# Performance work log

Measured on AMD Instinct MI355X. Metric: run time of the kernel, lower is better.

## Reference

```python
import jax, jax.numpy as jnp
import numpy as np

EMBED = 1024
B, S = 8, 2048

def setup_inputs() -> dict:
    key = jax.random.key(0)
    k1, k2 = jax.random.split(key)
    x = jax.random.normal(k1, (B, S, EMBED), dtype=jnp.float32)
    # torch Linear(embed, 3*embed): store weight already transposed as [E, 3E]
    W_qkv = jax.random.normal(k2, (EMBED, 3 * EMBED), dtype=jnp.float32) * (1.0 / np.sqrt(EMBED))
    b_qkv = jnp.zeros((3 * EMBED,), dtype=jnp.float32)
    return {"x": x, "W_qkv": W_qkv, "b_qkv": b_qkv}

def reference(x, W_qkv, b_qkv):
    E = x.shape[-1]
    qkv = x @ W_qkv + b_qkv                      # [B,S,3E]
    Q, K, V = jnp.split(qkv, 3, axis=-1)         # each [B,S,E]
    scale = 1.0 / jnp.sqrt(jnp.asarray(E, x.dtype))
    scores = jnp.einsum('bqe,bke->bqk', Q, K) * scale  # [B,S,S]
    attn = jax.nn.softmax(scores, axis=-1)
    return jnp.einsum('bqk,bke->bqe', attn, V)   # [B,S,E]
```

## Files before the change

### kernel.cpp

```cpp
#include <hip/hip_runtime.h>

typedef unsigned short u16;
typedef unsigned int u32;
typedef __attribute__((ext_vector_type(8))) short short8;
typedef __attribute__((ext_vector_type(4))) short short4v;
typedef __attribute__((ext_vector_type(4))) float f32x4;

__device__ __forceinline__ u16 f2bf(float f) {
    u32 u = __float_as_uint(f);
    u32 r = (u + 0x7fffu + ((u >> 16) & 1u)) >> 16;
    return (u16)r;
}
__device__ __forceinline__ float bf2f(u16 h) {
    return __uint_as_float(((u32)h) << 16);
}

__device__ __forceinline__ void gload_lds16(const void* g, void* l) {
    __builtin_amdgcn_global_load_lds((const __attribute__((address_space(1))) void*)g,
                                     (__attribute__((address_space(3))) void*)l, 16, 0, 0);
}

#define BARRIER() do { __builtin_amdgcn_sched_barrier(0); __builtin_amdgcn_s_barrier(); __builtin_amdgcn_sched_barrier(0); } while (0)
#define VMCNT(N)  asm volatile("s_waitcnt vmcnt(" #N ")" ::: "memory")


__device__ __forceinline__ void stage_half(const u16* __restrict__ gtile, int ldg, int kcol0,
                                           char* lds, int regionOff, int r0,
                                           int wid, int lane)
{
    const int cc = kcol0 + (((lane & 7) ^ (lane >> 3)) << 3);
    #pragma unroll
    for (int j = 0; j < 2; ++j) {
        const int rbase = r0 + j * 64 + (wid << 3);
        gload_lds16(gtile + (size_t)(rbase + (lane >> 3)) * ldg + cc,
                    lds + regionOff + (size_t)rbase * 128);
    }
}

template<int ROFF, int QH>
__device__ __forceinline__ void ld_a(short8 (&a)[4][2], const char* lds, int arow, const int colk[2]) {
    #pragma unroll
    for (int mf = 0; mf < 4; ++mf)
        #pragma unroll
        for (int kh = 0; kh < 2; ++kh)
            a[mf][kh] = *(const short8*)(lds + ROFF + QH * 16384 + mf * 2048 + arow + colk[kh]);
}
template<int ROFF, int QH>
__device__ __forceinline__ void ld_b(short8 (&b)[2][2], const char* lds, int brow, const int colk[2]) {
    #pragma unroll
    for (int nf = 0; nf < 2; ++nf)
        #pragma unroll
        for (int kh = 0; kh < 2; ++kh)
            b[nf][kh] = *(const short8*)(lds + ROFF + QH * 16384 + nf * 2048 + brow + colk[kh]);
}

template<int QM, int QN>
__device__ __forceinline__ void mfq(f32x4 (&acc)[2][4][2][2], short8 (&a)[4][2], short8 (&b)[2][2]) {
    __builtin_amdgcn_s_setprio(1);
    #pragma unroll
    for (int mf = 0; mf < 4; ++mf)
        #pragma unroll
        for (int nf = 0; nf < 2; ++nf) {
            acc[QM][mf][QN][nf] = __builtin_amdgcn_mfma_f32_16x16x32_bf16(a[mf][0], b[nf][0], acc[QM][mf][QN][nf], 0, 0, 0);
            acc[QM][mf][QN][nf] = __builtin_amdgcn_mfma_f32_16x16x32_bf16(a[mf][1], b[nf][1], acc[QM][mf][QN][nf], 0, 0, 0);
        }
    __builtin_amdgcn_s_setprio(0);
}

template<int EPI>
__global__ __launch_bounds__(512, 2)
void gemm8p(const u16* __restrict__ A, int lda, long long sA,
            const u16* __restrict__ B, int ldb, long long sB,
            void* __restrict__ Cv, int ldc, long long sC,
            const float* __restrict__ bias, float scale, int K)
{
    extern __shared__ char lds[];
    const int tid  = threadIdx.x;
    const int wid  = tid >> 6;
    const int lane = tid & 63;
    const long long z = blockIdx.z;

    const int bm = blockIdx.y * 256;
    const int bn = blockIdx.x * 256;
    const u16* Atile = A + z * sA + (size_t)bm * lda;
    const u16* Btile = B + z * sB + (size_t)bn * ldb;

    const int wm = wid >> 2;
    const int wn = wid & 3;

    const int l15  = lane & 15;
    const int lxor = (lane & 7) << 4;
    const int khi  = (lane >> 4) << 4;
    const int colk[2] = { khi ^ lxor, (64 + khi) ^ lxor };
    const int arow = (wm * 64 + l15) * 128;
    const int brow = (wn * 32 + l15) * 128;

    f32x4 acc[2][4][2][2];
    #pragma unroll
    for (int i = 0; i < 2; ++i)
        #pragma unroll
        for (int m = 0; m < 4; ++m)
            #pragma unroll
            for (int j = 0; j < 2; ++j)
                #pragma unroll
                for (int n = 0; n < 2; ++n)
                    acc[i][m][j][n] = (f32x4){0.f, 0.f, 0.f, 0.f};

    const int NT = K >> 6;
    const int NI = NT >> 1;

    stage_half(Atile, lda, 0,  lds, 0,     0,   wid, lane);
    stage_half(Btile, ldb, 0,  lds, 32768, 0,   wid, lane);
    stage_half(Atile, lda, 0,  lds, 0,     128, wid, lane);
    stage_half(Btile, ldb, 0,  lds, 32768, 128, wid, lane);
    stage_half(Atile, lda, 64, lds, 65536, 0,   wid, lane);
    stage_half(Btile, ldb, 64, lds, 98304, 0,   wid, lane);
    VMCNT(4);
    BARRIER();

    short8 a[4][2], b[2][2];

    for (int it = 0; it < NI; ++it) {
        const int k1 = (2 * it + 1) << 6;
        const int k2 = (2 * it + 2) << 6;
        const int k3 = (2 * it + 3) << 6;
        const bool lastit = (it == NI - 1);

        ld_a<0, 0>(a, lds, arow, colk);
        ld_b<32768, 0>(b, lds, brow, colk);
        stage_half(Atile, lda, k1, lds, 65536, 128, wid, lane);
        BARRIER(); mfq<0, 0>(acc, a, b); BARRIER();
        ld_b<32768, 1>(b, lds, brow, colk);
        stage_half(Btile, ldb, k1, lds, 98304, 128, wid, lane);
        BARRIER(); mfq<0, 1>(acc, a, b); BARRIER();
        ld_a<0, 1>(a, lds, arow, colk);
        ld_b<32768, 0>(b, lds, brow, colk);
        if (!lastit) stage_half(Atile, lda, k2, lds, 0, 0, wid, lane);
        BARRIER(); mfq<1, 0>(acc, a, b); BARRIER();
        ld_b<32768, 1>(b, lds, brow, colk);
        if (!lastit) { stage_half(Btile, ldb, k2, lds, 32768, 0, wid, lane); VMCNT(4); }
        else         { VMCNT(0); }
        BARRIER(); mfq<1, 1>(acc, a, b); BARRIER();
        ld_a<65536, 0>(a, lds, arow, colk);
        ld_b<98304, 0>(b, lds, brow, colk);
        if (!lastit) stage_half(Atile, lda, k2, lds, 0, 128, wid, lane);
        BARRIER(); mfq<0, 0>(acc, a, b); BARRIER();
        ld_b<98304, 1>(b, lds, brow, colk);
        if (!lastit) stage_half(Btile, ldb, k2, lds, 32768, 128, wid, lane);
        BARRIER(); mfq<0, 1>(acc, a, b); BARRIER();
        ld_a<65536, 1>(a, lds, arow, colk);
        ld_b<98304, 0>(b, lds, brow, colk);
        if (!lastit) stage_half(Atile, lda, k3, lds, 65536, 0, wid, lane);
        BARRIER(); mfq<1, 0>(acc, a, b); BARRIER();
        ld_b<98304, 1>(b, lds, brow, colk);
        if (!lastit) { stage_half(Btile, ldb, k3, lds, 98304, 0, wid, lane); VMCNT(4); }
        BARRIER(); mfq<1, 1>(acc, a, b); BARRIER();
    }

    const int r0 = (lane >> 4) * 4;
    const int cc = lane & 15;
    #pragma unroll
    for (int qn = 0; qn < 2; ++qn)
        #pragma unroll
        for (int nf = 0; nf < 2; ++nf) {
            const int col = bn + qn * 128 + wn * 32 + nf * 16 + cc;
            const float badd = (EPI == 0) ? bias[col] : 0.f;
            #pragma unroll
            for (int qm = 0; qm < 2; ++qm)
                #pragma unroll
                for (int mf = 0; mf < 4; ++mf) {
                    const int row = bm + qm * 128 + wm * 64 + mf * 16 + r0;
                    #pragma unroll
                    for (int r = 0; r < 4; ++r) {
                        const float v = acc[qm][mf][qn][nf][r] * scale + badd;
                        if (EPI == 2) ((float*)Cv + z * sC)[(size_t)(row + r) * ldc + col] = v;
                        else          ((u16*)Cv + z * sC)[(size_t)(row + r) * ldc + col] = f2bf(v);
                    }
                }
        }
}

__global__ __launch_bounds__(256)
void cvt_f32_bf16(const float* __restrict__ in, u16* __restrict__ out, int n8)
{
    const int i = blockIdx.x * 256 + threadIdx.x;
    if (i >= n8) return;
    const float4* p = (const float4*)in;
    const float4 a = p[2 * i], b = p[2 * i + 1];
    short8 o;
    o[0] = (short)f2bf(a.x); o[1] = (short)f2bf(a.y);
    o[2] = (short)f2bf(a.z); o[3] = (short)f2bf(a.w);
    o[4] = (short)f2bf(b.x); o[5] = (short)f2bf(b.y);
    o[6] = (short)f2bf(b.z); o[7] = (short)f2bf(b.w);
    ((short8*)out)[i] = o;
}

__global__ __launch_bounds__(256)
void cvt_w_t(const float* __restrict__ W, u16* __restrict__ Wt)
{
    __shared__ u16 T[32][33];
    const int tid = threadIdx.x;
    const int tr = tid >> 3;
    const int tc = (tid & 7) * 4;
    const int c0 = blockIdx.x * 32;
    const int r0 = blockIdx.y * 32;
    const float4 v = *(const float4*)&W[(size_t)(r0 + tr) * 3072 + c0 + tc];
    T[tr][tc + 0] = f2bf(v.x); T[tr][tc + 1] = f2bf(v.y);
    T[tr][tc + 2] = f2bf(v.z); T[tr][tc + 3] = f2bf(v.w);
    __syncthreads();
    short4v o;
    o[0] = (short)T[tc + 0][tr]; o[1] = (short)T[tc + 1][tr];
    o[2] = (short)T[tc + 2][tr]; o[3] = (short)T[tc + 3][tr];
    *(short4v*)&Wt[(size_t)(c0 + tr) * 1024 + r0 + tc] = o;
}

__global__ __launch_bounds__(256)
void trans_v(const u16* __restrict__ qkv, u16* __restrict__ Vt)
{
    __shared__ u16 T[32][33];
    const int tid = threadIdx.x;
    const int tr = tid >> 3;
    const int tc = (tid & 7) * 4;
    const int e0 = blockIdx.x * 32;
    const int s0 = blockIdx.y * 32;
    const int b  = blockIdx.z;
    const short4v v = *(const short4v*)&qkv[(size_t)(b * 2048 + s0 + tr) * 3072 + 2048 + e0 + tc];
    T[tr][tc + 0] = (u16)v[0]; T[tr][tc + 1] = (u16)v[1];
    T[tr][tc + 2] = (u16)v[2]; T[tr][tc + 3] = (u16)v[3];
    __syncthreads();
    short4v o;
    o[0] = (short)T[tc + 0][tr]; o[1] = (short)T[tc + 1][tr];
    o[2] = (short)T[tc + 2][tr]; o[3] = (short)T[tc + 3][tr];
    *(short4v*)&Vt[(size_t)b * 1024 * 2048 + (size_t)(e0 + tr) * 2048 + s0 + tc] = o;
}

__global__ __launch_bounds__(256)
void softmax_bf16(u16* __restrict__ S)
{
    u16* row = S + (size_t)blockIdx.x * 2048;
    const int tid  = threadIdx.x;
    const int wid  = tid >> 6;
    const int lane = tid & 63;
    __shared__ float red[4];

    const short8 v8 = *(const short8*)&row[tid * 8];
    float v[8];
    float m = -3.4e38f;
    #pragma unroll
    for (int j = 0; j < 8; ++j) { v[j] = bf2f((u16)v8[j]); m = fmaxf(m, v[j]); }
    #pragma unroll
    for (int off = 32; off; off >>= 1) m = fmaxf(m, __shfl_xor(m, off));
    if (lane == 0) red[wid] = m;
    __syncthreads();
    m = fmaxf(fmaxf(red[0], red[1]), fmaxf(red[2], red[3]));
    float s = 0.f;
    #pragma unroll
    for (int j = 0; j < 8; ++j) { v[j] = __expf(v[j] - m); s += v[j]; }
    #pragma unroll
    for (int off = 32; off; off >>= 1) s += __shfl_xor(s, off);
    __syncthreads();
    if (lane == 0) red[wid] = s;
    __syncthreads();
    s = red[0] + red[1] + red[2] + red[3];
    const float inv = 1.f / s;
    short8 o;
    #pragma unroll
    for (int j = 0; j < 8; ++j) o[j] = (short)f2bf(v[j] * inv);
    *(short8*)&row[tid * 8] = o;
}

extern "C" void kernel_launch(void* const* d_in, const int* in_sizes, int n_in,
                              void* d_out, int out_size, void* d_ws, size_t ws_size,
                              hipStream_t stream) {
    const float* x    = (const float*)d_in[0];
    const float* W    = (const float*)d_in[1];
    const float* bias = (const float*)d_in[2];
    float* out = (float*)d_out;

    const int B = 8, S = 2048, E = 1024, N3 = 3072;
    const int M = B * S;

    char* ws = (char*)d_ws;
    u16* xb   = (u16*)ws;
    u16* Wtb  = (u16*)(ws + 33554432);
    u16* qkvb = (u16*)(ws + 39845888);
    u16* Vtb  = (u16*)(ws + 140509184);
    u16* Sb   = (u16*)(ws + 174063616);

    const size_t need_full = 174063616ull + (size_t)B * S * S * 2;
    const bool full = ws_size >= need_full;
    const float sc = 1.0f / 32.0f;
    const int LDSB = 131072;

    (void)hipFuncSetAttribute(reinterpret_cast<const void*>(&gemm8p<0>),
                              hipFuncAttributeMaxDynamicSharedMemorySize, LDSB);
    (void)hipFuncSetAttribute(reinterpret_cast<const void*>(&gemm8p<1>),
                              hipFuncAttributeMaxDynamicSharedMemorySize, LDSB);
    (void)hipFuncSetAttribute(reinterpret_cast<const void*>(&gemm8p<2>),
                              hipFuncAttributeMaxDynamicSharedMemorySize, LDSB);

    cvt_f32_bf16<<<dim3((M * E) / 8 / 256), 256, 0, stream>>>(x, xb, (M * E) / 8);
    cvt_w_t<<<dim3(96, 32), 256, 0, stream>>>(W, Wtb);

    gemm8p<0><<<dim3(N3 / 256, M / 256, 1), 512, LDSB, stream>>>(
        xb, E, 0, Wtb, E, 0, qkvb, N3, 0, bias, 1.0f, E);

    trans_v<<<dim3(32, 64, 8), 256, 0, stream>>>(qkvb, Vtb);

    if (full) {
        gemm8p<1><<<dim3(S / 256, S / 256, 8), 512, LDSB, stream>>>(
            qkvb, N3, (long long)S * N3, qkvb + E, N3, (long long)S * N3,
            Sb, S, (long long)S * S, nullptr, sc, E);
        softmax_bf16<<<dim3(B * S), 256, 0, stream>>>(Sb);
        gemm8p<2><<<dim3(E / 256, S / 256, 8), 512, LDSB, stream>>>(
            Sb, S, (long long)S * S, Vtb, S, (long long)E * S,
            out, E, (long long)S * E, nullptr, 1.0f, S);
    } else {
        for (int b = 0; b < B; ++b) {
            const u16* Qb = qkvb + (size_t)b * S * N3;
            gemm8p<1><<<dim3(S / 256, S / 256, 1), 512, LDSB, stream>>>(
                Qb, N3, 0, Qb + E, N3, 0, Sb, S, 0, nullptr, sc, E);
            softmax_bf16<<<dim3(S), 256, 0, stream>>>(Sb);
            gemm8p<2><<<dim3(E / 256, S / 256, 1), 512, LDSB, stream>>>(
                Sb, S, 0, Vtb + (size_t)b * E * S, S, 0,
                out + (size_t)b * S * E, E, 0, nullptr, 1.0f, S);
        }
    }
}
```

Before: 314.0 us.

## Rework GEMM prefetch schedule, template strides, and remap blocks across XCDs

The GEMM kernel's K-loop is restructured so each iteration covers 128 K and prefetches a whole 64-K stage at once (deeper vmcnt(8)). It keeps two B fragment registers so the quadrant order can reuse loaded B. Leading dimensions and K become template constants, and per-lane global pointers are precomputed to cut address arithmetic. A 1D grid with an XCD-aware block remap (bid&7 interleave) is meant to improve L2 locality on the multi-die MI355X. The costs are more registers per thread and a more intricate barrier and wait schedule that must stay correct.

New measurement: 292.7 us. 6.8% less time.

```diff
diff --git a/kernel.cpp b/kernel.cpp
--- a/kernel.cpp
+++ b/kernel.cpp
@@ -23,35 +23,25 @@
 #define BARRIER() do { __builtin_amdgcn_sched_barrier(0); __builtin_amdgcn_s_barrier(); __builtin_amdgcn_sched_barrier(0); } while (0)
 #define VMCNT(N)  asm volatile("s_waitcnt vmcnt(" #N ")" ::: "memory")
 
-
-__device__ __forceinline__ void stage_half(const u16* __restrict__ gtile, int ldg, int kcol0,
-                                           char* lds, int regionOff, int r0,
-                                           int wid, int lane)
-{
-    const int cc = kcol0 + (((lane & 7) ^ (lane >> 3)) << 3);
-    #pragma unroll
-    for (int j = 0; j < 2; ++j) {
-        const int rbase = r0 + j * 64 + (wid << 3);
-        gload_lds16(gtile + (size_t)(rbase + (lane >> 3)) * ldg + cc,
-                    lds + regionOff + (size_t)rbase * 128);
+#define STAGE(ptr, LDG, LOFF, RBASE, kelem) \
+    do { gload_lds16((ptr) + (size_t)(RBASE) * (LDG) + (kelem),        lds + (LOFF) + ((RBASE) + (wid << 3)) * 128); \
+         gload_lds16((ptr) + (size_t)((RBASE) + 64) * (LDG) + (kelem), lds + (LOFF) + ((RBASE) + 64 + (wid << 3)) * 128); } while (0)
+
+template<int ROFF, int QH>
+__device__ __forceinline__ void ld_a(short8 (&a)[4][2], const char* lds, int arow, int c0, int c1) {
+    #pragma unroll
+    for (int mf = 0; mf < 4; ++mf) {
+        a[mf][0] = *(const short8*)(lds + ROFF + QH * 16384 + mf * 2048 + arow + c0);
+        a[mf][1] = *(const short8*)(lds + ROFF + QH * 16384 + mf * 2048 + arow + c1);
     }
 }
-
 template<int ROFF, int QH>
-__device__ __forceinline__ void ld_a(short8 (&a)[4][2], const char* lds, int arow, const int colk[2]) {
-    #pragma unroll
-    for (int mf = 0; mf < 4; ++mf)
-        #pragma unroll
-        for (int kh = 0; kh < 2; ++kh)
-            a[mf][kh] = *(const short8*)(lds + ROFF + QH * 16384 + mf * 2048 + arow + colk[kh]);
-}
-template<int ROFF, int QH>
-__device__ __forceinline__ void ld_b(short8 (&b)[2][2], const char* lds, int brow, const int colk[2]) {
-    #pragma unroll
-    for (int nf = 0; nf < 2; ++nf)
-        #pragma unroll
-        for (int kh = 0; kh < 2; ++kh)
-            b[nf][kh] = *(const short8*)(lds + ROFF + QH * 16384 + nf * 2048 + brow + colk[kh]);
+__device__ __forceinline__ void ld_b(short8 (&b)[2][2], const char* lds, int brow, int c0, int c1) {
+    #pragma unroll
+    for (int nf = 0; nf < 2; ++nf) {
+        b[nf][0] = *(const short8*)(lds + ROFF + QH * 16384 + nf * 2048 + brow + c0);
+        b[nf][1] = *(const short8*)(lds + ROFF + QH * 16384 + nf * 2048 + brow + c1);
+    }
 }
 
 template<int QM, int QN>
@@ -67,33 +57,43 @@
     __builtin_amdgcn_s_setprio(0);
 }
 
-template<int EPI>
+template<int EPI, int LDA, int LDB, int LDC, int K>
 __global__ __launch_bounds__(512, 2)
-void gemm8p(const u16* __restrict__ A, int lda, long long sA,
-            const u16* __restrict__ B, int ldb, long long sB,
-            void* __restrict__ Cv, int ldc, long long sC,
-            const float* __restrict__ bias, float scale, int K)
+void gemm8p(const u16* __restrict__ A, long long sA,
+            const u16* __restrict__ B, long long sB,
+            void* __restrict__ Cv, long long sC,
+            const float* __restrict__ bias, float scale,
+            int GX, int GY)
 {
     extern __shared__ char lds[];
     const int tid  = threadIdx.x;
     const int wid  = tid >> 6;
     const int lane = tid & 63;
-    const long long z = blockIdx.z;
-
-    const int bm = blockIdx.y * 256;
-    const int bn = blockIdx.x * 256;
-    const u16* Atile = A + z * sA + (size_t)bm * lda;
-    const u16* Btile = B + z * sB + (size_t)bn * ldb;
-
-    const int wm = wid >> 2;
-    const int wn = wid & 3;
-
-    const int l15  = lane & 15;
-    const int lxor = (lane & 7) << 4;
-    const int khi  = (lane >> 4) << 4;
-    const int colk[2] = { khi ^ lxor, (64 + khi) ^ lxor };
-    const int arow = (wm * 64 + l15) * 128;
-    const int brow = (wn * 32 + l15) * 128;
+
+    const int nwg = gridDim.x;
+    int bid = blockIdx.x;
+    bid = (bid & 7) * (nwg >> 3) + (bid >> 3);
+    const int bx  = bid % GX;
+    const int rem = bid / GX;
+    const int by  = rem % GY;
+    const long long z = rem / GY;
+
+    const int bm = by * 256, bn = bx * 256;
+    const u16* Atile = A + z * sA + (size_t)bm * LDA;
+    const u16* Btile = B + z * sB + (size_t)bn * LDB;
+
+    const int wm = wid >> 2, wn = wid & 3;
+    const int l15   = lane & 15;
+    const int lxor  = (lane & 7) << 4;
+    const int khi   = (lane >> 4) << 4;
+    const int colk0 = khi ^ lxor;
+    const int colk1 = (64 + khi) ^ lxor;
+    const int arow  = (wm * 64 + l15) * 128;
+    const int brow  = (wn * 32 + l15) * 128;
+
+    const int swz = ((lane & 7) ^ (lane >> 3)) << 3;
+    const u16* pA = Atile + (size_t)((wid << 3) + (lane >> 3)) * LDA + swz;
+    const u16* pB = Btile + (size_t)((wid << 3) + (lane >> 3)) * LDB + swz;
 
     f32x4 acc[2][4][2][2];
     #pragma unroll
@@ -106,55 +106,42 @@
                 for (int n = 0; n < 2; ++n)
                     acc[i][m][j][n] = (f32x4){0.f, 0.f, 0.f, 0.f};
 
-    const int NT = K >> 6;
-    const int NI = NT >> 1;
-
-    stage_half(Atile, lda, 0,  lds, 0,     0,   wid, lane);
-    stage_half(Btile, ldb, 0,  lds, 32768, 0,   wid, lane);
-    stage_half(Atile, lda, 0,  lds, 0,     128, wid, lane);
-    stage_half(Btile, ldb, 0,  lds, 32768, 128, wid, lane);
-    stage_half(Atile, lda, 64, lds, 65536, 0,   wid, lane);
-    stage_half(Btile, ldb, 64, lds, 98304, 0,   wid, lane);
-    VMCNT(4);
+    STAGE(pA, LDA, 0,     0,   0);  STAGE(pB, LDB, 32768, 0,   0);
+    STAGE(pA, LDA, 0,     128, 0);  STAGE(pB, LDB, 32768, 128, 0);
+    STAGE(pB, LDB, 98304, 0,   64); STAGE(pA, LDA, 65536, 0,   64);
+    STAGE(pB, LDB, 98304, 128, 64); STAGE(pA, LDA, 65536, 128, 64);
+    VMCNT(8);
     BARRIER();
 
-    short8 a[4][2], b[2][2];
+    short8 a[4][2], b0[2][2], b1[2][2];
+    const int NI = K >> 7;
 
     for (int it = 0; it < NI; ++it) {
-        const int k1 = (2 * it + 1) << 6;
-        const int k2 = (2 * it + 2) << 6;
-        const int k3 = (2 * it + 3) << 6;
-        const bool lastit = (it == NI - 1);
-
-        ld_a<0, 0>(a, lds, arow, colk);
-        ld_b<32768, 0>(b, lds, brow, colk);
-        stage_half(Atile, lda, k1, lds, 65536, 128, wid, lane);
-        BARRIER(); mfq<0, 0>(acc, a, b); BARRIER();
-        ld_b<32768, 1>(b, lds, brow, colk);
-        stage_half(Btile, ldb, k1, lds, 98304, 128, wid, lane);
-        BARRIER(); mfq<0, 1>(acc, a, b); BARRIER();
-        ld_a<0, 1>(a, lds, arow, colk);
-        ld_b<32768, 0>(b, lds, brow, colk);
-        if (!lastit) stage_half(Atile, lda, k2, lds, 0, 0, wid, lane);
-        BARRIER(); mfq<1, 0>(acc, a, b); BARRIER();
-        ld_b<32768, 1>(b, lds, brow, colk);
-        if (!lastit) { stage_half(Btile, ldb, k2, lds, 32768, 0, wid, lane); VMCNT(4); }
-        else         { VMCNT(0); }
-        BARRIER(); mfq<1, 1>(acc, a, b); BARRIER();
-        ld_a<65536, 0>(a, lds, arow, colk);
-        ld_b<98304, 0>(b, lds, brow, colk);
-        if (!lastit) stage_half(Atile, lda, k2, lds, 0, 128, wid, lane);
-        BARRIER(); mfq<0, 0>(acc, a, b); BARRIER();
-        ld_b<98304, 1>(b, lds, brow, colk);
-        if (!lastit) stage_half(Btile, ldb, k2, lds, 32768, 128, wid, lane);
-        BARRIER(); mfq<0, 1>(acc, a, b); BARRIER();
-        ld_a<65536, 1>(a, lds, arow, colk);
-        ld_b<98304, 0>(b, lds, brow, colk);
-        if (!lastit) stage_half(Atile, lda, k3, lds, 65536, 0, wid, lane);
-        BARRIER(); mfq<1, 0>(acc, a, b); BARRIER();
-        ld_b<98304, 1>(b, lds, brow, colk);
-        if (!lastit) { stage_half(Btile, ldb, k3, lds, 98304, 0, wid, lane); VMCNT(4); }
-        BARRIER(); mfq<1, 1>(acc, a, b); BARRIER();
+        const bool more = (it + 1 < NI);
+        const int kn = it * 128 + 128;
+        ld_a<0, 0>(a, lds, arow, colk0, colk1);
+        ld_b<32768, 0>(b0, lds, brow, colk0, colk1);
+        BARRIER(); mfq<0, 0>(acc, a, b0); BARRIER();
+        ld_b<32768, 1>(b1, lds, brow, colk0, colk1);
+        if (more) STAGE(pB, LDB, 32768, 0, kn);
+        BARRIER(); mfq<0, 1>(acc, a, b1); BARRIER();
+        ld_a<0, 1>(a, lds, arow, colk0, colk1);
+        if (more) STAGE(pA, LDA, 0, 0, kn);
+        BARRIER(); mfq<1, 1>(acc, a, b1); BARRIER();
+        if (more) { STAGE(pB, LDB, 32768, 128, kn); STAGE(pA, LDA, 0, 128, kn); VMCNT(8); }
+        else      { VMCNT(0); }
+        BARRIER(); mfq<1, 0>(acc, a, b0); BARRIER();
+        ld_a<65536, 0>(a, lds, arow, colk0, colk1);
+        ld_b<98304, 0>(b0, lds, brow, colk0, colk1);
+        BARRIER(); mfq<0, 0>(acc, a, b0); BARRIER();
+        ld_b<98304, 1>(b1, lds, brow, colk0, colk1);
+        if (more) STAGE(pB, LDB, 98304, 0, kn + 64);
+        BARRIER(); mfq<0, 1>(acc, a, b1); BARRIER();
+        ld_a<65536, 1>(a, lds, arow, colk0, colk1);
+        if (more) STAGE(pA, LDA, 65536, 0, kn + 64);
+        BARRIER(); mfq<1, 1>(acc, a, b1); BARRIER();
+        if (more) { STAGE(pB, LDB, 98304, 128, kn + 64); STAGE(pA, LDA, 65536, 128, kn + 64); VMCNT(8); }
+        BARRIER(); mfq<1, 0>(acc, a, b0); BARRIER();
     }
 
     const int r0 = (lane >> 4) * 4;
@@ -173,8 +160,8 @@
                     #pragma unroll
                     for (int r = 0; r < 4; ++r) {
                         const float v = acc[qm][mf][qn][nf][r] * scale + badd;
-                        if (EPI == 2) ((float*)Cv + z * sC)[(size_t)(row + r) * ldc + col] = v;
-                        else          ((u16*)Cv + z * sC)[(size_t)(row + r) * ldc + col] = f2bf(v);
+                        if (EPI == 2) ((float*)Cv + z * sC)[(size_t)(row + r) * LDC + col] = v;
+                        else          ((u16*)Cv + z * sC)[(size_t)(row + r) * LDC + col] = f2bf(v);
                     }
                 }
         }
@@ -292,38 +279,40 @@
     const float sc = 1.0f / 32.0f;
     const int LDSB = 131072;
 
-    (void)hipFuncSetAttribute(reinterpret_cast<const void*>(&gemm8p<0>),
+    auto kQKV = gemm8p<0, 1024, 1024, 3072, 1024>;
+    auto kQKT = gemm8p<1, 3072, 3072, 2048, 1024>;
+    auto kPV  = gemm8p<2, 2048, 2048, 1024, 2048>;
+    (void)hipFuncSetAttribute(reinterpret_cast<const void*>(kQKV),
                               hipFuncAttributeMaxDynamicSharedMemorySize, LDSB);
-    (void)hipFuncSetAttribute(reinterpret_cast<const void*>(&gemm8p<1>),
+    (void)hipFuncSetAttribute(reinterpret_cast<const void*>(kQKT),
                               hipFuncAttributeMaxDynamicSharedMemorySize, LDSB);
-    (void)hipFuncSetAttribute(reinterpret_cast<const void*>(&gemm8p<2>),
+    (void)hipFuncSetAttribute(reinterpret_cast<const void*>(kPV),
                               hipFuncAttributeMaxDynamicSharedMemorySize, LDSB);
 
     cvt_f32_bf16<<<dim3((M * E) / 8 / 256), 256, 0, stream>>>(x, xb, (M * E) / 8);
     cvt_w_t<<<dim3(96, 32), 256, 0, stream>>>(W, Wtb);
 
-    gemm8p<0><<<dim3(N3 / 256, M / 256, 1), 512, LDSB, stream>>>(
-        xb, E, 0, Wtb, E, 0, qkvb, N3, 0, bias, 1.0f, E);
+    kQKV<<<dim3(12 * 64), 512, LDSB, stream>>>(xb, 0, Wtb, 0, qkvb, 0, bias, 1.0f, 12, 64);
 
     trans_v<<<dim3(32, 64, 8), 256, 0, stream>>>(qkvb, Vtb);
 
     if (full) {
-        gemm8p<1><<<dim3(S / 256, S / 256, 8), 512, LDSB, stream>>>(
-            qkvb, N3, (long long)S * N3, qkvb + E, N3, (long long)S * N3,
-            Sb, S, (long long)S * S, nullptr, sc, E);
+        kQKT<<<dim3(8 * 8 * 8), 512, LDSB, stream>>>(
+            qkvb, (long long)S * N3, qkvb + E, (long long)S * N3,
+            Sb, (long long)S * S, nullptr, sc, 8, 8);
         softmax_bf16<<<dim3(B * S), 256, 0, stream>>>(Sb);
-        gemm8p<2><<<dim3(E / 256, S / 256, 8), 512, LDSB, stream>>>(
-            Sb, S, (long long)S * S, Vtb, S, (long long)E * S,
-            out, E, (long long)S * E, nullptr, 1.0f, S);
+        kPV<<<dim3(4 * 8 * 8), 512, LDSB, stream>>>(
+            Sb, (long long)S * S, Vtb, (long long)E * S,
+            out, (long long)S * E, nullptr, 1.0f, 4, 8);
     } else {
         for (int b = 0; b < B; ++b) {
             const u16* Qb = qkvb + (size_t)b * S * N3;
-            gemm8p<1><<<dim3(S / 256, S / 256, 1), 512, LDSB, stream>>>(
-                Qb, N3, 0, Qb + E, N3, 0, Sb, S, 0, nullptr, sc, E);
+            kQKT<<<dim3(8 * 8), 512, LDSB, stream>>>(
+                Qb, 0, Qb + E, 0, Sb, 0, nullptr, sc, 8, 8);
             softmax_bf16<<<dim3(S), 256, 0, stream>>>(Sb);
-            gemm8p<2><<<dim3(E / 256, S / 256, 1), 512, LDSB, stream>>>(
-                Sb, S, 0, Vtb + (size_t)b * E * S, S, 0,
-                out + (size_t)b * S * E, E, 0, nullptr, 1.0f, S);
+            kPV<<<dim3(4 * 8), 512, LDSB, stream>>>(
+                Sb, 0, Vtb + (size_t)b * E * S, 0,
+                out + (size_t)b * S * E, 0, nullptr, 1.0f, 4, 8);
         }
     }
 }
```
